# Performance work log

Measured on AMD Instinct MI355X. Metric: run time of the kernel, lower is better.

## Reference

```python
import jax, jax.numpy as jnp
import numpy as np
from jax import lax

NHEAD = 8
DC = 32
BN_EPS = 1e-5


def setup_inputs() -> dict:
    key = jax.random.key(0)
    ks = jax.random.split(key, 8)
    b, t, h, w = 8, 128, 32, 64
    l = h * w
    prev_attn = jax.random.uniform(ks[0], (b * NHEAD, t, l), dtype=jnp.float32)
    curr_attn = jax.random.uniform(ks[1], (b * NHEAD, t, l), dtype=jnp.float32)
    key_padding_mask = jax.random.bernoulli(ks[2], 0.2, (b, l))  # True = padded
    conv_w = jax.random.normal(ks[3], (DC, 2 * NHEAD, 5, 5), dtype=jnp.float32) * 0.05
    conv_b = jnp.zeros((DC,), dtype=jnp.float32)
    proj_w = jax.random.normal(ks[4], (NHEAD, DC, 1, 1), dtype=jnp.float32) * 0.1
    bn_gamma = jnp.ones((NHEAD,), dtype=jnp.float32)
    bn_beta = jnp.zeros((NHEAD,), dtype=jnp.float32)
    return {"prev_attn": prev_attn, "curr_attn": curr_attn,
            "key_padding_mask": key_padding_mask, "h": 32,
            "conv_w": conv_w, "conv_b": conv_b, "proj_w": proj_w,
            "bn_gamma": bn_gamma, "bn_beta": bn_beta}


def _forward(prev_attn, curr_attn, conv_w, conv_b, proj_w, bn_gamma, bn_beta,
             key_padding_mask, h):
    b, l = key_padding_mask.shape
    t = curr_attn.shape[1]
    w = l // h
    n = NHEAD
    prev = prev_attn.reshape(b, n, t, l)
    curr = curr_attn.reshape(b, n, t, l)
    attns = jnp.concatenate([prev, curr], axis=1)            # (b, 2n, t, l)
    attns = jnp.cumsum(attns, axis=2) - attns                # exclusive cumsum over t
    # 'b n t (h w) -> (b t) n h w'
    attns = attns.transpose(0, 2, 1, 3).reshape(b * t, 2 * n, h, w)
    cov = lax.conv_general_dilated(attns, conv_w, (1, 1), [(2, 2), (2, 2)],
                                   dimension_numbers=("NCHW", "OIHW", "NCHW"))
    cov = jax.nn.relu(cov + conv_b[None, :, None, None])
    # mask: 'b (h w) -> (b t) 1 h w'
    mask = jnp.broadcast_to(key_padding_mask.reshape(b, 1, 1, h, w),
                            (b, t, 1, h, w)).reshape(b * t, 1, h, w)
    cov = jnp.where(mask, 0.0, cov)
    # 1x1 conv, no bias
    cov = jnp.einsum("bdhw,nd->bnhw", cov, proj_w[:, :, 0, 0])  # (bt, n, h, w)
    # MaskBatchNorm2d: BN over unmasked pixels (training-mode batch stats)
    nm = (~mask).astype(cov.dtype)                              # (bt, 1, h, w)
    cnt = jnp.maximum(nm.sum(), 1.0)
    mean = (cov * nm).sum(axis=(0, 2, 3)) / cnt                 # (n,)
    diff = cov - mean[None, :, None, None]
    var = (diff * diff * nm).sum(axis=(0, 2, 3)) / cnt          # biased var
    y = bn_gamma[None, :, None, None] * diff * lax.rsqrt(var + BN_EPS)[None, :, None, None] \
        + bn_beta[None, :, None, None]
    cov = jnp.where(mask, cov, y)
    # '(b t) n h w -> (b n) t (h w)'
    cov = cov.reshape(b, t, n, h * w).transpose(0, 2, 1, 3).reshape(b * n, t, h * w)
    return cov


def reference(prev_attn, curr_attn, key_padding_mask, h,
              conv_w, conv_b, proj_w, bn_gamma, bn_beta):
    return _forward(prev_attn, curr_attn, conv_w, conv_b, proj_w,
                    bn_gamma, bn_beta, key_padding_mask, h)
```

## Files before the change

### kernel.cpp

```cpp
#include <hip/hip_runtime.h>
#include <hip/hip_bf16.h>


typedef __attribute__((ext_vector_type(4))) float f32x4;
typedef __attribute__((ext_vector_type(8))) short short8;
typedef __attribute__((ext_vector_type(8))) unsigned short u16x8;

#define B_   8
#define NH   8
#define T_   128
#define H_   32
#define W_   64
#define L_   2048
#define CIN  16
#define DCC  32
#define WSTR 420

__device__ __forceinline__ unsigned short f2h(float f){
  _Float16 h = (_Float16)f;
  return __builtin_bit_cast(unsigned short, h);
}
__device__ __forceinline__ float h2f(unsigned short u){
  _Float16 h = __builtin_bit_cast(_Float16, u);
  return (float)h;
}
__device__ __forceinline__ unsigned pkrtz(float a, float b){
  return __builtin_bit_cast(unsigned, __builtin_amdgcn_cvt_pkrtz(a, b));
}
__device__ __forceinline__ int swz(int a){ return a ^ ((a >> 3) & 0x30); }

__global__ void k_front(const float* __restrict__ prev,
                        const float* __restrict__ curr,
                        uint2* __restrict__ cum2,
                        const float* __restrict__ convw,
                        const float* __restrict__ projw,
                        const void* __restrict__ mraw,
                        unsigned short* __restrict__ Wt,
                        unsigned short* __restrict__ Pt,
                        unsigned char* __restrict__ mB,
                        float* __restrict__ cntOut)
{
  int tid = threadIdx.x;
  int blk = blockIdx.x;
  if (blk < 256){
    int gid = blk * 256 + tid;
    int p4 = gid & 511;
    int ci = (gid >> 9) & 15;
    int b  = gid >> 13;
    const float* src = ((ci < 8)
        ? prev + ((size_t)(b*8 + ci) * T_) * L_
        : curr + ((size_t)(b*8 + ci - 8) * T_) * L_) + p4*4;
    uint2* dst = cum2 + ((size_t)(b*CIN + ci) * T_) * (L_/4) + p4;
    float a0 = 0.f, a1 = 0.f, a2 = 0.f, a3 = 0.f;
    #pragma unroll 4
    for (int t = 0; t < T_; t++){
      uint2 o;
      o.x = (unsigned)f2h(a0) | ((unsigned)f2h(a1) << 16);
      o.y = (unsigned)f2h(a2) | ((unsigned)f2h(a3) << 16);
      dst[(size_t)t * (L_/4)] = o;
      f32x4 v = *(const f32x4*)(src + (size_t)t * L_);
      a0 += v.x; a1 += v.y; a2 += v.z; a3 += v.w;
    }
    return;
  }
  int blk2 = blk - 256;
  if (blk2 < 32){
    int co = blk2;
    for (int k = tid; k < WSTR; k += 256){
      float v = 0.f;
      if (k < 416){
        int g  = k >> 5, kk = k & 31;
        int kb = kk >> 3, j = kk & 7;
        int ci = (kb & 1)*8 + j;
        int h  = kb >> 1;
        int dy, dx, valid = 1;
        if (g < 10){ dx = g >> 1; dy = (g & 1)*2 + h; }
        else { dy = 4; dx = 2*(g - 10) + h; if (dx > 4) valid = 0; }
        if (valid) v = convw[(((co*CIN + ci)*5 + dy)*5) + dx];
      }
      Wt[co*WSTR + k] = f2h(v);
    }
  } else if (blk2 == 32){
    for (int idx = tid; idx < 16*32; idx += 256){
      int n = idx >> 5, q = idx & 31;
      float v = (n < 8) ? projw[n*32 + 16*(q & 1) + (q >> 1)] : 0.f;
      Pt[idx] = f2h(v);
    }
  } else {
    __shared__ int s_flags;
    __shared__ int s_cnt;
    if (tid == 0){ s_flags = 0; s_cnt = 0; }
    __syncthreads();
    const unsigned* w = (const unsigned*)mraw;
    int fl = 0;
    for (int i = tid; i < 4096; i += 256){
      unsigned v = w[i];
      if (v == 0x3F800000u) fl |= 2;
      else if (v > 1u)      fl |= 1;
      else if (v == 1u)     fl |= 4;
    }
    if (fl) atomicOr(&s_flags, fl);
    __syncthreads();
    int flags = s_flags;
    int mode = (flags & 1) ? 0 : ((flags & 2) ? 2 : ((flags & 4) ? 1 : 0));
    int c = 0;
    int base = (blk2 - 33) * 1024;
    for (int k = 0; k < 4; k++){
      int i = base + k*256 + tid;
      int m;
      if (mode == 0)      m = (((const unsigned char*)mraw)[i] != 0);
      else if (mode == 2) m = (((const float*)mraw)[i] != 0.f);
      else                m = (((const int*)mraw)[i] != 0);
      mB[i] = (unsigned char)m;
      c += 1 - m;
    }
    atomicAdd(&s_cnt, c);
    __syncthreads();
    if (tid == 0) atomicAdd(cntOut, 128.0f * (float)s_cnt);
  }
}

__global__ __launch_bounds__(256, 3) void k_conv(
    const unsigned short* __restrict__ cumIn,
    const unsigned short* __restrict__ Wt,
    const unsigned short* __restrict__ Pt,
    const unsigned char* __restrict__ mB,
    const float* __restrict__ convb,
    unsigned short* __restrict__ cov,
    float* __restrict__ slots)
{
  __shared__ alignas(16) unsigned short img[20*68*16];
  __shared__ alignas(16) unsigned short plds[16*32];
  __shared__ alignas(16) unsigned sval[4][16*20];
  __shared__ unsigned long long mbl[16];

  const int tid  = threadIdx.x;
  const int bid  = blockIdx.x;
  const int half = bid & 1;
  const int bt   = bid >> 1;
  const int t    = bt & 127;
  const int b    = bt >> 7;
  const int ylo  = half * 16;
  const int lane = tid & 63;
  const int wv   = tid >> 6;
  const int mrow = lane & 15;
  const int kb   = lane >> 4;

  if (wv == 0){
    #pragma unroll
    for (int k2 = 0; k2 < 16; k2++){
      int m = mB[b*L_ + half*1024 + k2*64 + lane];
      unsigned long long bal = __ballot(m != 0);
      if (lane == 0) mbl[k2] = bal;
    }
  } else if (wv == 1){
    const uint4* srcp = (const uint4*)Pt;
    uint4* dstp = (uint4*)plds;
    for (int i = lane; i < 64; i += 64) dstp[i] = srcp[i];
  }

  for (int it = tid; it < 640; it += 256){
    int cp  = it & 7;
    int xxi = (it >> 3) & 3;
    int yy  = it >> 5;
    int xx  = (xxi < 2) ? xxi : 64 + xxi;
    int ad  = ((yy*68 + xx)*16 + 2*cp)*2;
    *(unsigned*)((char*)img + swz(ad)) = 0u;
  }
  #pragma unroll
  for (int iter = 0; iter < 5; iter++){
    int it = iter*256 + tid;
    int xc = it & 7;
    int cp = (it >> 3) & 7;
    int yy = it >> 6;
    int y  = ylo - 2 + yy;
    uint4 r0 = (uint4){0,0,0,0}, r1 = (uint4){0,0,0,0};
    if (y >= 0 && y < H_){
      const unsigned short* rp = cumIn + (((size_t)(b*CIN + 2*cp) * T_ + t) * L_) + y*W_ + xc*8;
      r0 = *(const uint4*)rp;
      r1 = *(const uint4*)(rp + (size_t)T_ * L_);
    }
    int sbase = ((yy*68 + 2 + xc*8)*16 + 2*cp)*2;
    unsigned rr0[4] = {r0.x, r0.y, r0.z, r0.w};
    unsigned rr1[4] = {r1.x, r1.y, r1.z, r1.w};
    #pragma unroll
    for (int d = 0; d < 4; d++){
      unsigned wl = __builtin_amdgcn_perm(rr1[d], rr0[d], 0x05040100u);
      unsigned wh = __builtin_amdgcn_perm(rr1[d], rr0[d], 0x07060302u);
      *(unsigned*)((char*)img + swz(sbase + (2*d  )*32)) = wl;
      *(unsigned*)((char*)img + swz(sbase + (2*d+1)*32)) = wh;
    }
  }
  __syncthreads();

  const float cb0 = convb[mrow];
  const float cb1 = convb[mrow + 16];
  const short8 pbf = *(const short8*)&plds[mrow*32 + kb*8];
  const unsigned short* Wg = Wt + mrow*WSTR + kb*8;
  const char* imgc = (const char*)img;

  int offs_[13];
  {
    const int h = kb >> 1;
    #pragma unroll
    for (int g = 0; g < 13; g++){
      int dy, dx;
      if (g < 10){ dx = g >> 1; dy = (g & 1)*2 + h; }
      else { dy = 4; dx = 2*(g - 10) + h; if (dx > 4) dx = 4; }
      offs_[g] = (dy*68 + dx)*32 + (kb & 1)*16;
    }
  }

  float ssum = 0.f, ssq = 0.f;

  #pragma unroll 1
  for (int c = 0; c < 2; c++){
    int wofs = 0;
    asm volatile("" : "+v"(wofs));
    const int pbase = wv*256 + c*128;
    const unsigned long long mw0 = mbl[(pbase >> 6)];
    const unsigned long long mw1 = mbl[(pbase >> 6) + 1];
    const int base_u = ((pbase >> 6)*68 + mrow)*32;
    f32x4 acc[8][2];
    #pragma unroll
    for (int mt = 0; mt < 8; mt++){ acc[mt][0] = (f32x4)0.f; acc[mt][1] = (f32x4)0.f; }

    short8 bfa_c = *(const short8*)(Wg + wofs);
    short8 bfb_c = *(const short8*)(Wg + wofs + 6720);
    #pragma unroll
    for (int ks = 0; ks < 13; ks++){
      short8 bfa_n = bfa_c, bfb_n = bfb_c;
      if (ks < 12){
        bfa_n = *(const short8*)(Wg + wofs + (ks+1)*32);
        bfb_n = *(const short8*)(Wg + wofs + 6720 + (ks+1)*32);
      }
      const char* p0 = imgc + swz(base_u + offs_[ks]);
      const char* p1 = imgc + swz(base_u + 2176 + offs_[ks]);
      short8 a[8];
      a[0] = *(const short8*)(p0);
      a[1] = *(const short8*)(p0 + 512);
      a[2] = *(const short8*)(p0 + 1024);
      a[3] = *(const short8*)(p0 + 1536);
      a[4] = *(const short8*)(p1);
      a[5] = *(const short8*)(p1 + 512);
      a[6] = *(const short8*)(p1 + 1024);
      a[7] = *(const short8*)(p1 + 1536);
      #pragma unroll
      for (int mt = 0; mt < 8; mt++){
        acc[mt][0] = __builtin_amdgcn_mfma_f32_16x16x32_f16(a[mt], bfa_c, acc[mt][0], 0, 0, 0);
        acc[mt][1] = __builtin_amdgcn_mfma_f32_16x16x32_f16(a[mt], bfb_c, acc[mt][1], 0, 0, 0);
      }
      bfa_c = bfa_n; bfb_c = bfb_n;
    }

    unsigned* sv = &sval[wv][0];
    #pragma unroll
    for (int mt = 0; mt <= 8; mt++){
      if (mt >= 1){
        const int m = mt - 1;
        short8 pa = *(const short8*)&sv[mrow*20 + kb*4];
        f32x4 pc = (f32x4)0.f;
        pc = __builtin_amdgcn_mfma_f32_16x16x32_f16(pa, pbf, pc, 0, 0, 0);
        if (mrow < 8){
          const unsigned long long mwm = (m < 4) ? mw0 : mw1;
          size_t covbase = (((size_t)bt*NH + mrow) * L_) + half*1024 + pbase + m*16 + kb*4;
          uint2 st;
          st.x = pkrtz(pc[0], pc[1]);
          st.y = pkrtz(pc[2], pc[3]);
          *(uint2*)&cov[covbase] = st;
          #pragma unroll
          for (int r = 0; r < 4; r++){
            int bi = (m*16 + kb*4 + r) & 63;
            if (!((mwm >> bi) & 1)){ ssum += pc[r]; ssq += pc[r]*pc[r]; }
          }
        }
      }
      if (mt < 8){
        const unsigned long long mw = (mt < 4) ? mw0 : mw1;
        #pragma unroll
        for (int r = 0; r < 4; r += 2){
          int bi0 = (mt*16 + kb*4 + r)     & 63;
          int bi1 = (mt*16 + kb*4 + r + 1) & 63;
          float v0a = fmaxf(acc[mt][0][r]   + cb0, 0.f);
          float v1a = fmaxf(acc[mt][1][r]   + cb1, 0.f);
          float v0b = fmaxf(acc[mt][0][r+1] + cb0, 0.f);
          float v1b = fmaxf(acc[mt][1][r+1] + cb1, 0.f);
          if ((mw >> bi0) & 1){ v0a = 0.f; v1a = 0.f; }
          if ((mw >> bi1) & 1){ v0b = 0.f; v1b = 0.f; }
          sv[(kb*4 + r    )*20 + mrow] = pkrtz(v0a, v1a);
          sv[(kb*4 + r + 1)*20 + mrow] = pkrtz(v0b, v1b);
        }
      }
    }
  }

  ssum += __shfl_xor(ssum, 16);
  ssum += __shfl_xor(ssum, 32);
  ssq  += __shfl_xor(ssq, 16);
  ssq  += __shfl_xor(ssq, 32);
  if (lane < 8){
    atomicAdd(&slots[(bid & 7)*16 + lane],     ssum);
    atomicAdd(&slots[(bid & 7)*16 + 8 + lane], ssq);
  }
}

__global__ void k_stats(const float* __restrict__ slots,
                        const float* __restrict__ cntp,
                        const float* __restrict__ gamma,
                        const float* __restrict__ beta,
                        float* __restrict__ ab)
{
  int tid = threadIdx.x;
  if (tid < 8){
    double s = 0.0, q = 0.0;
    for (int i = 0; i < 8; i++){
      s += (double)slots[i*16 + tid];
      q += (double)slots[i*16 + 8 + tid];
    }
    double cnt  = (double)fmaxf(*cntp, 1.0f);
    double mean = s / cnt;
    double var  = q / cnt - mean*mean;
    float inv = (float)(1.0 / sqrt(var + 1e-5));
    float A = gamma[tid] * inv;
    float Bc = beta[tid] - (float)mean * A;
    ab[tid]     = A;
    ab[8 + tid] = Bc;
  }
}

__global__ void k_out(const unsigned short* __restrict__ cov,
                      const unsigned char* __restrict__ mB,
                      const float* __restrict__ ab,
                      float* __restrict__ out)
{
  size_t gid = (size_t)blockIdx.x * 256 + threadIdx.x;
  size_t e = gid * 8;
  int px = (int)(e & 2047);
  size_t r = e >> 11;
  int t = (int)(r & 127); r >>= 7;
  int n = (int)(r & 7);
  int b = (int)(r >> 3);
  const unsigned short* cp = cov + ((((size_t)b*T_ + t)*NH + n) << 11) + px;
  u16x8 cv = *(const u16x8*)cp;
  unsigned long long mm = *(const unsigned long long*)(mB + (size_t)b*L_ + px);
  float A = ab[n], Bc = ab[8 + n];
  float res[8];
  #pragma unroll
  for (int j = 0; j < 8; j++){
    float v = h2f(cv[j]);
    res[j] = ((mm >> (8*j)) & 0xFFull) ? v : (A*v + Bc);
  }
  f32x4* o = (f32x4*)(out + e);
  o[0] = (f32x4){res[0], res[1], res[2], res[3]};
  o[1] = (f32x4){res[4], res[5], res[6], res[7]};
}

extern "C" void kernel_launch(void* const* d_in, const int* in_sizes, int n_in,
                              void* d_out, int out_size, void* d_ws, size_t ws_size,
                              hipStream_t stream)
{
  const float* prev  = (const float*)d_in[0];
  const float* curr  = (const float*)d_in[1];
  const void*  mraw  = d_in[2];
  const float* convw = (const float*)d_in[4];
  const float* convb = (const float*)d_in[5];
  const float* projw = (const float*)d_in[6];
  const float* gamma = (const float*)d_in[7];
  const float* beta  = (const float*)d_in[8];
  float* out = (float*)d_out;

  char* ws = (char*)d_ws;
  unsigned short* cumIn = (unsigned short*)(ws);
  unsigned short* cov   = (unsigned short*)(ws + 67108864);
  unsigned char*  mB    = (unsigned char*) (ws + 100663296);
  unsigned short* Wt    = (unsigned short*)(ws + 100679680);
  unsigned short* Pt    = (unsigned short*)(ws + 100706560);
  float* slots          = (float*)(ws + 100707584);
  float* cntp           = (float*)(ws + 100708096);
  float* ab             = (float*)(ws + 100708160);
  if (ws_size < (size_t)100708224) return;

  hipMemsetAsync(slots, 0, 640, stream);
  k_front <<<305,  256, 0, stream>>>(prev, curr, (uint2*)cumIn,
                                     convw, projw, mraw, Wt, Pt, mB, cntp);
  k_conv  <<<2048, 256, 0, stream>>>(cumIn, Wt, Pt, mB, convb, cov, slots);
  k_stats <<<1,    64,  0, stream>>>(slots, cntp, gamma, beta, ab);
  k_out   <<<8192, 256, 0, stream>>>(cov, mB, ab, out);
}
```

Baseline: 174.4 us.

## Preload conv weights into registers and double-buffer LDS image fragments

The conv kernel now loads all 13 weight fragments per output group into registers once, before the barrier, so their global latency overlaps the LDS fill. Inside the K loop it prefetches the next step's image fragments from LDS while MFMAs run, with s_setprio raised around the MFMA block. Tap offsets move into a constant table. The extra registers lead to lowering launch bounds from 3 to 2 waves per SIMD, which cuts occupancy in exchange for better latency hiding.

```diff
diff --git a/kernel.cpp b/kernel.cpp
--- a/kernel.cpp
+++ b/kernel.cpp
@@ -120,7 +120,10 @@
   }
 }
 
-__global__ __launch_bounds__(256, 3) void k_conv(
+__device__ __constant__ const int kCg[13] =
+  {0, 4352, 32, 4384, 64, 4416, 96, 4448, 128, 4480, 8704, 8768, 8832};
+
+__global__ __launch_bounds__(256, 2) void k_conv(
     const unsigned short* __restrict__ cumIn,
     const unsigned short* __restrict__ Wt,
     const unsigned short* __restrict__ Pt,
@@ -191,7 +194,6 @@
       *(unsigned*)((char*)img + swz(sbase + (2*d+1)*32)) = wh;
     }
   }
-  __syncthreads();
 
   const float cb0 = convb[mrow];
   const float cb1 = convb[mrow + 16];
@@ -199,58 +201,71 @@
   const unsigned short* Wg = Wt + mrow*WSTR + kb*8;
   const char* imgc = (const char*)img;
 
-  int offs_[13];
-  {
-    const int h = kb >> 1;
-    #pragma unroll
-    for (int g = 0; g < 13; g++){
-      int dy, dx;
-      if (g < 10){ dx = g >> 1; dy = (g & 1)*2 + h; }
-      else { dy = 4; dx = 2*(g - 10) + h; if (dx > 4) dx = 4; }
-      offs_[g] = (dy*68 + dx)*32 + (kb & 1)*16;
-    }
-  }
+  short8 wA[13], wB[13];
+  #pragma unroll
+  for (int ks = 0; ks < 13; ks++){
+    wA[ks] = *(const short8*)(Wg + ks*32);
+    wB[ks] = *(const short8*)(Wg + 6720 + ks*32);
+  }
+  __syncthreads();
+
+  const int h  = kb >> 1;
+  const int lo = (kb & 1)*16;
+  const int rA = h*2176 + lo;
+  const int rB = h*32   + lo;
+  const int rC = lo;
 
   float ssum = 0.f, ssq = 0.f;
 
   #pragma unroll 1
   for (int c = 0; c < 2; c++){
-    int wofs = 0;
-    asm volatile("" : "+v"(wofs));
     const int pbase = wv*256 + c*128;
     const unsigned long long mw0 = mbl[(pbase >> 6)];
     const unsigned long long mw1 = mbl[(pbase >> 6) + 1];
     const int base_u = ((pbase >> 6)*68 + mrow)*32;
+    const int bA = base_u + rA, bB = base_u + rB, bC = base_u + rC;
     f32x4 acc[8][2];
     #pragma unroll
     for (int mt = 0; mt < 8; mt++){ acc[mt][0] = (f32x4)0.f; acc[mt][1] = (f32x4)0.f; }
 
-    short8 bfa_c = *(const short8*)(Wg + wofs);
-    short8 bfb_c = *(const short8*)(Wg + wofs + 6720);
+    short8 av[8], nv[8];
+    {
+      const char* p0 = imgc + swz(bA + kCg[0]);
+      const char* p1 = imgc + swz(bA + kCg[0] + 2176);
+      av[0] = *(const short8*)(p0);
+      av[1] = *(const short8*)(p0 + 512);
+      av[2] = *(const short8*)(p0 + 1024);
+      av[3] = *(const short8*)(p0 + 1536);
+      av[4] = *(const short8*)(p1);
+      av[5] = *(const short8*)(p1 + 512);
+      av[6] = *(const short8*)(p1 + 1024);
+      av[7] = *(const short8*)(p1 + 1536);
+    }
     #pragma unroll
     for (int ks = 0; ks < 13; ks++){
-      short8 bfa_n = bfa_c, bfb_n = bfb_c;
       if (ks < 12){
-        bfa_n = *(const short8*)(Wg + wofs + (ks+1)*32);
-        bfb_n = *(const short8*)(Wg + wofs + 6720 + (ks+1)*32);
+        const int g1 = ks + 1;
+        const int u  = (g1 < 10 ? bA : (g1 < 12 ? bB : bC)) + kCg[g1];
+        const char* q0 = imgc + swz(u);
+        const char* q1 = imgc + swz(u + 2176);
+        nv[0] = *(const short8*)(q0);
+        nv[1] = *(const short8*)(q0 + 512);
+        nv[2] = *(const short8*)(q0 + 1024);
+        nv[3] = *(const short8*)(q0 + 1536);
+        nv[4] = *(const short8*)(q1);
+        nv[5] = *(const short8*)(q1 + 512);
+        nv[6] = *(const short8*)(q1 + 1024);
+        nv[7] = *(const short8*)(q1 + 1536);
       }
-      const char* p0 = imgc + swz(base_u + offs_[ks]);
-      const char* p1 = imgc + swz(base_u + 2176 + offs_[ks]);
-      short8 a[8];
-      a[0] = *(const short8*)(p0);
-      a[1] = *(const short8*)(p0 + 512);
-      a[2] = *(const short8*)(p0 + 1024);
-      a[3] = *(const short8*)(p0 + 1536);
-      a[4] = *(const short8*)(p1);
-      a[5] = *(const short8*)(p1 + 512);
-      a[6] = *(const short8*)(p1 + 1024);
-      a[7] = *(const short8*)(p1 + 1536);
+      __builtin_amdgcn_s_setprio(1);
       #pragma unroll
       for (int mt = 0; mt < 8; mt++){
-        acc[mt][0] = __builtin_amdgcn_mfma_f32_16x16x32_f16(a[mt], bfa_c, acc[mt][0], 0, 0, 0);
-        acc[mt][1] = __builtin_amdgcn_mfma_f32_16x16x32_f16(a[mt], bfb_c, acc[mt][1], 0, 0, 0);
+        acc[mt][0] = __builtin_amdgcn_mfma_f32_16x16x32_f16(av[mt], wA[ks], acc[mt][0], 0, 0, 0);
+        acc[mt][1] = __builtin_amdgcn_mfma_f32_16x16x32_f16(av[mt], wB[ks], acc[mt][1], 0, 0, 0);
       }
-      bfa_c = bfa_n; bfb_c = bfb_n;
+      __builtin_amdgcn_s_setprio(0);
+      #pragma unroll
+      for (int i = 0; i < 8; i++) av[i] = nv[i];
     }
 
     unsigned* sv = &sval[wv][0];
```

New measurement: 189.6 us. 8.7% more time.

## Split cumsum across more threads and stagger conv k-steps across waves

Applied to the files above, without the earlier changes.

The prefix-sum front kernel now has each thread handle 2 columns instead of 4, which doubles the block count to expose more memory parallelism. In the conv kernel the explicit software prefetch of weight fragments is removed. Each k-step now loads its weights directly, wraps its MFMA burst in s_setprio, and odd waves start at a different k-step than even waves, so waves sharing a SIMD interleave their LDS reads and MFMAs. The trade-off is narrower global accesses in the cumsum and possibly less latency hiding for the weight loads.

```diff
diff --git a/kernel.cpp b/kernel.cpp
--- a/kernel.cpp
+++ b/kernel.cpp
@@ -3,6 +3,7 @@
 
 
 typedef __attribute__((ext_vector_type(4))) float f32x4;
+typedef __attribute__((ext_vector_type(2))) float f32x2;
 typedef __attribute__((ext_vector_type(8))) short short8;
 typedef __attribute__((ext_vector_type(8))) unsigned short u16x8;
 
@@ -31,7 +32,7 @@
 
 __global__ void k_front(const float* __restrict__ prev,
                         const float* __restrict__ curr,
-                        uint2* __restrict__ cum2,
+                        unsigned* __restrict__ cum1,
                         const float* __restrict__ convw,
                         const float* __restrict__ projw,
                         const void* __restrict__ mraw,
@@ -42,28 +43,25 @@
 {
   int tid = threadIdx.x;
   int blk = blockIdx.x;
-  if (blk < 256){
+  if (blk < 512){
     int gid = blk * 256 + tid;
-    int p4 = gid & 511;
-    int ci = (gid >> 9) & 15;
-    int b  = gid >> 13;
+    int p2 = gid & 1023;
+    int ci = (gid >> 10) & 15;
+    int b  = gid >> 14;
     const float* src = ((ci < 8)
         ? prev + ((size_t)(b*8 + ci) * T_) * L_
-        : curr + ((size_t)(b*8 + ci - 8) * T_) * L_) + p4*4;
-    uint2* dst = cum2 + ((size_t)(b*CIN + ci) * T_) * (L_/4) + p4;
-    float a0 = 0.f, a1 = 0.f, a2 = 0.f, a3 = 0.f;
-    #pragma unroll 4
+        : curr + ((size_t)(b*8 + ci - 8) * T_) * L_) + p2*2;
+    unsigned* dst = cum1 + ((size_t)(b*CIN + ci) * T_) * (L_/2) + p2;
+    float a0 = 0.f, a1 = 0.f;
+    #pragma unroll 8
     for (int t = 0; t < T_; t++){
-      uint2 o;
-      o.x = (unsigned)f2h(a0) | ((unsigned)f2h(a1) << 16);
-      o.y = (unsigned)f2h(a2) | ((unsigned)f2h(a3) << 16);
-      dst[(size_t)t * (L_/4)] = o;
-      f32x4 v = *(const f32x4*)(src + (size_t)t * L_);
-      a0 += v.x; a1 += v.y; a2 += v.z; a3 += v.w;
+      dst[(size_t)t * (L_/2)] = (unsigned)f2h(a0) | ((unsigned)f2h(a1) << 16);
+      f32x2 v = *(const f32x2*)(src + (size_t)t * L_);
+      a0 += v.x; a1 += v.y;
     }
     return;
   }
-  int blk2 = blk - 256;
+  int blk2 = blk - 512;
   if (blk2 < 32){
     int co = blk2;
     for (int k = tid; k < WSTR; k += 256){
@@ -225,33 +223,37 @@
     #pragma unroll
     for (int mt = 0; mt < 8; mt++){ acc[mt][0] = (f32x4)0.f; acc[mt][1] = (f32x4)0.f; }
 
-    short8 bfa_c = *(const short8*)(Wg + wofs);
-    short8 bfb_c = *(const short8*)(Wg + wofs + 6720);
-    #pragma unroll
-    for (int ks = 0; ks < 13; ks++){
-      short8 bfa_n = bfa_c, bfb_n = bfb_c;
-      if (ks < 12){
-        bfa_n = *(const short8*)(Wg + wofs + (ks+1)*32);
-        bfb_n = *(const short8*)(Wg + wofs + 6720 + (ks+1)*32);
-      }
-      const char* p0 = imgc + swz(base_u + offs_[ks]);
-      const char* p1 = imgc + swz(base_u + 2176 + offs_[ks]);
-      short8 a[8];
-      a[0] = *(const short8*)(p0);
-      a[1] = *(const short8*)(p0 + 512);
-      a[2] = *(const short8*)(p0 + 1024);
-      a[3] = *(const short8*)(p0 + 1536);
-      a[4] = *(const short8*)(p1);
-      a[5] = *(const short8*)(p1 + 512);
-      a[6] = *(const short8*)(p1 + 1024);
-      a[7] = *(const short8*)(p1 + 1536);
-      #pragma unroll
-      for (int mt = 0; mt < 8; mt++){
-        acc[mt][0] = __builtin_amdgcn_mfma_f32_16x16x32_f16(a[mt], bfa_c, acc[mt][0], 0, 0, 0);
-        acc[mt][1] = __builtin_amdgcn_mfma_f32_16x16x32_f16(a[mt], bfb_c, acc[mt][1], 0, 0, 0);
-      }
-      bfa_c = bfa_n; bfb_c = bfb_n;
-    }
+    #define KSTEP(ks) do { \
+      short8 bfa = *(const short8*)(Wg + wofs + (ks)*32); \
+      short8 bfb = *(const short8*)(Wg + wofs + 6720 + (ks)*32); \
+      const char* p0 = imgc + swz(base_u + offs_[(ks)]); \
+      const char* p1 = imgc + swz(base_u + 2176 + offs_[(ks)]); \
+      short8 a[8]; \
+      a[0] = *(const short8*)(p0); \
+      a[1] = *(const short8*)(p0 + 512); \
+      a[2] = *(const short8*)(p0 + 1024); \
+      a[3] = *(const short8*)(p0 + 1536); \
+      a[4] = *(const short8*)(p1); \
+      a[5] = *(const short8*)(p1 + 512); \
+      a[6] = *(const short8*)(p1 + 1024); \
+      a[7] = *(const short8*)(p1 + 1536); \
+      __builtin_amdgcn_s_setprio(1); \
+      _Pragma("unroll") \
+      for (int mt = 0; mt < 8; mt++){ \
+        acc[mt][0] = __builtin_amdgcn_mfma_f32_16x16x32_f16(a[mt], bfa, acc[mt][0], 0, 0, 0); \
+        acc[mt][1] = __builtin_amdgcn_mfma_f32_16x16x32_f16(a[mt], bfb, acc[mt][1], 0, 0, 0); \
+      } \
+      __builtin_amdgcn_s_setprio(0); \
+    } while (0)
+
+    if ((wv & 1) == 0){
+      KSTEP(0); KSTEP(1); KSTEP(2); KSTEP(3); KSTEP(4); KSTEP(5); KSTEP(6);
+      KSTEP(7); KSTEP(8); KSTEP(9); KSTEP(10); KSTEP(11); KSTEP(12);
+    } else {
+      KSTEP(6); KSTEP(7); KSTEP(8); KSTEP(9); KSTEP(10); KSTEP(11); KSTEP(12);
+      KSTEP(0); KSTEP(1); KSTEP(2); KSTEP(3); KSTEP(4); KSTEP(5);
+    }
+    #undef KSTEP
 
     unsigned* sv = &sval[wv][0];
     #pragma unroll
@@ -381,7 +383,7 @@
   if (ws_size < (size_t)100708224) return;
 
   hipMemsetAsync(slots, 0, 640, stream);
-  k_front <<<305,  256, 0, stream>>>(prev, curr, (uint2*)cumIn,
+  k_front <<<561,  256, 0, stream>>>(prev, curr, (unsigned*)cumIn,
                                      convw, projw, mraw, Wt, Pt, mB, cntp);
   k_conv  <<<2048, 256, 0, stream>>>(cumIn, Wt, Pt, mB, convb, cov, slots);
   k_stats <<<1,    64,  0, stream>>>(slots, cntp, gamma, beta, ab);
```

Measured after the change: 183.9 us. 5.5% more time.
